# Performance work log

Hardware: AMD Instinct MI355X
Metric: run time of the kernel (lower is better)

Reference implementation:

```python
import jax, jax.numpy as jnp
import numpy as np

N, E = 40000, 640000
EMB, HID, H, TXT = 128, 128, 4, 384
C = HID // H  # per-head channels = 32


def _prelu(x, a):
    return jnp.where(x >= 0, x, a * x)


def _layernorm(x, g, b, eps=1e-5):
    m = jnp.mean(x, axis=-1, keepdims=True)
    v = jnp.mean((x - m) ** 2, axis=-1, keepdims=True)
    return (x - m) / jnp.sqrt(v + eps) * g + b


def _gat_conv(h, src, dst, W, att_src, att_dst, bias):
    # PyG GATConv (concat=True, eval mode): lin has no bias, self-loops already in src/dst.
    xh = (h @ W.T).reshape(N, H, C)                      # [N,H,C]
    a_src = jnp.sum(xh * att_src, axis=-1)               # [N,H]
    a_dst = jnp.sum(xh * att_dst, axis=-1)               # [N,H]
    alpha = jax.nn.leaky_relu(a_src[src] + a_dst[dst], negative_slope=0.2)  # [Et,H]
    amax = jax.ops.segment_max(alpha, dst, num_segments=N)
    ex = jnp.exp(alpha - amax[dst])
    denom = jax.ops.segment_sum(ex, dst, num_segments=N)
    coef = ex / denom[dst]                               # scatter-softmax over dst
    out = jax.ops.segment_sum(xh[src] * coef[:, :, None], dst, num_segments=N)
    return out.reshape(N, H * C) + bias


def setup_inputs() -> dict:
    key = jax.random.key(0)
    ks = jax.random.split(key, 20)
    nrm = lambda k, s, sc=0.05: jax.random.normal(k, s, jnp.float32) * sc
    inp = {
        "x": nrm(ks[0], (N, EMB), 1.0),
        "num_x": nrm(ks[1], (N, 1), 1.0),
        "num_mask": jnp.ones((N,), jnp.float32),
        "txt_x": nrm(ks[2], (N, TXT), 1.0),
        "txt_mask": jnp.ones((N,), jnp.float32),
        "edge_index": jax.random.randint(ks[3], (2, E), 0, N, jnp.int32),
        "num_proj_w": nrm(ks[4], (EMB, 1)), "num_proj_b": jnp.zeros((EMB,), jnp.float32),
        "txt_proj_w": nrm(ks[5], (EMB, TXT)), "txt_proj_b": jnp.zeros((EMB,), jnp.float32),
        "node_proj_w": nrm(ks[6], (HID, EMB)), "node_proj_b": jnp.zeros((HID,), jnp.float32),
        "prelu0_a": jnp.full((HID,), 0.25, jnp.float32),
        "conv1_w": nrm(ks[7], (HID, HID)), "att_src1": nrm(ks[8], (H, C)), "att_dst1": nrm(ks[9], (H, C)), "bias1": jnp.zeros((HID,), jnp.float32),
        "norm1_g": jnp.ones((HID,), jnp.float32), "norm1_b": jnp.zeros((HID,), jnp.float32),
        "prelu1_a": jnp.full((HID,), 0.25, jnp.float32),
        "conv2_w": nrm(ks[10], (HID, HID)), "att_src2": nrm(ks[11], (H, C)), "att_dst2": nrm(ks[12], (H, C)), "bias2": jnp.zeros((HID,), jnp.float32),
        "norm2_g": jnp.ones((HID,), jnp.float32), "norm2_b": jnp.zeros((HID,), jnp.float32),
        "prelu2_a": jnp.full((HID,), 0.25, jnp.float32),
        "out_w": nrm(ks[13], (1, HID)), "out_b": jnp.zeros((1,), jnp.float32),
    }
    return inp


def reference(x, num_x, num_mask, txt_x, txt_mask, edge_index,
              num_proj_w, num_proj_b, txt_proj_w, txt_proj_b,
              node_proj_w, node_proj_b, prelu0_a,
              conv1_w, att_src1, att_dst1, bias1, norm1_g, norm1_b, prelu1_a,
              conv2_w, att_src2, att_dst2, bias2, norm2_g, norm2_b, prelu2_a,
              out_w, out_b):
    # add self loops (PyG GATConv default)
    loop = jnp.arange(N, dtype=edge_index.dtype)
    src = jnp.concatenate([edge_index[0], loop])
    dst = jnp.concatenate([edge_index[1], loop])

    h = (num_x * num_mask[:, None]) @ num_proj_w.T + num_proj_b
    h = h + (txt_x * txt_mask[:, None]) @ txt_proj_w.T + txt_proj_b
    h = h + x @ node_proj_w.T + node_proj_b
    h = _prelu(h, prelu0_a)

    h = _gat_conv(h, src, dst, conv1_w, att_src1, att_dst1, bias1)
    h = _prelu(_layernorm(h, norm1_g, norm1_b), prelu1_a)  # dropout: eval mode -> identity

    h = _gat_conv(h, src, dst, conv2_w, att_src2, att_dst2, bias2)
    h = _prelu(_layernorm(h, norm2_g, norm2_b), prelu2_a)

    return (h @ out_w.T + out_b).squeeze(-1)  # [N]
```

## Files before the change

### kernel.cpp

```cpp
#include <hip/hip_runtime.h>
#include <stdint.h>

typedef unsigned short u16;
typedef unsigned int u32;
typedef __attribute__((ext_vector_type(8))) short bf16x8;
typedef __attribute__((ext_vector_type(4))) float f32x4;

__device__ __forceinline__ float bf2f(u32 u) {
    union { u32 i; float f; } v; v.i = u << 16; return v.f;
}
__device__ __forceinline__ u16 f2bf(float f) {
    u32 x = __float_as_uint(f);
    return (u16)((x + 0x7fffu + ((x >> 16) & 1u)) >> 16);
}
__device__ __forceinline__ float wred_sum(float v) {
#pragma unroll
    for (int o = 32; o > 0; o >>= 1) v += __shfl_xor(v, o, 64);
    return v;
}
__device__ __forceinline__ float wred_max(float v) {
#pragma unroll
    for (int o = 32; o > 0; o >>= 1) v = fmaxf(v, __shfl_xor(v, o, 64));
    return v;
}
__device__ __forceinline__ bf16x8 ldA_f32(const float* p, size_t off) {
    union { uint4 u; bf16x8 b; } t;
    const float* af = p + off;
    float4 a = *(const float4*)af, b2 = *(const float4*)(af + 4);
    t.u.x = (u32)f2bf(a.x)  | ((u32)f2bf(a.y)  << 16);
    t.u.y = (u32)f2bf(a.z)  | ((u32)f2bf(a.w)  << 16);
    t.u.z = (u32)f2bf(b2.x) | ((u32)f2bf(b2.y) << 16);
    t.u.w = (u32)f2bf(b2.z) | ((u32)f2bf(b2.w) << 16);
    return t.b;
}
__device__ __forceinline__ bf16x8 ld16B(const u16* p, size_t off) {
    union { uint4 u; bf16x8 b; } t; t.u = *(const uint4*)(p + off); return t.b;
}
__device__ __forceinline__ bf16x8 ldB(const u16* sw, int ct, int ks, int l16, int quad) {
    union { uint4 u; bf16x8 b; } t;
    t.u = *(const uint4*)&sw[(ct * 16 + l16) * 136 + ks * 32 + quad * 8];
    return t.b;
}
__device__ __forceinline__ void stage128(const float* W, int stride, int koff, u16* sw, int tid) {
#pragma unroll
    for (int it = 0; it < 16; ++it) {
        int idx = (it * 128 + tid) * 8;
        int c = idx >> 7, kk = idx & 127;
        const float* wf = W + (size_t)c * stride + koff + kk;
        float4 a = *(const float4*)wf, b = *(const float4*)(wf + 4);
        uint4 v;
        v.x = (u32)f2bf(a.x) | ((u32)f2bf(a.y) << 16);
        v.y = (u32)f2bf(a.z) | ((u32)f2bf(a.w) << 16);
        v.z = (u32)f2bf(b.x) | ((u32)f2bf(b.y) << 16);
        v.w = (u32)f2bf(b.z) | ((u32)f2bf(b.w) << 16);
        *(uint4*)&sw[c * 136 + kk] = v;
    }
}

__global__ void k_zero(int* __restrict__ p, int n) {
    int i = blockIdx.x * 256 + threadIdx.x;
    if (i < n) p[i] = 0;
}
__global__ void k_hist(const int* __restrict__ dst, int E, int* __restrict__ deg) {
    int e = blockIdx.x * 256 + threadIdx.x;
    if (e < E) atomicAdd(&deg[dst[e]], 1);
}
__global__ __launch_bounds__(1024) void k_scanA(const int* __restrict__ deg, int n,
                                                int* __restrict__ out, int* __restrict__ bsum) {
    __shared__ int wsum[16];
    int t = threadIdx.x, w = t >> 6, lane = t & 63;
    int i0 = blockIdx.x * 4096 + t * 4;
    int4 v = make_int4(0, 0, 0, 0);
    if (i0 + 3 < n) v = *(const int4*)&deg[i0];
    else {
        if (i0 < n)     v.x = deg[i0];
        if (i0 + 1 < n) v.y = deg[i0 + 1];
        if (i0 + 2 < n) v.z = deg[i0 + 2];
    }
    int tsum = v.x + v.y + v.z + v.w;
    int s = tsum;
#pragma unroll
    for (int o = 1; o < 64; o <<= 1) { int u = __shfl_up(s, o, 64); if (lane >= o) s += u; }
    if (lane == 63) wsum[w] = s;
    __syncthreads();
    if (w == 0 && lane < 16) {
        int ws = wsum[lane];
#pragma unroll
        for (int o = 1; o < 16; o <<= 1) { int u = __shfl_up(ws, o, 64); if (lane >= o) ws += u; }
        wsum[lane] = ws;
    }
    __syncthreads();
    int woff = (w == 0) ? 0 : wsum[w - 1];
    int p = woff + s - tsum;
    if (i0 + 3 < n) {
        int4 o4; o4.x = p; o4.y = p + v.x; o4.z = p + v.x + v.y; o4.w = p + v.x + v.y + v.z;
        *(int4*)&out[i0] = o4;
    } else {
        int pp = p;
        if (i0 < n)     { out[i0] = pp;     pp += v.x; }
        if (i0 + 1 < n) { out[i0 + 1] = pp; pp += v.y; }
        if (i0 + 2 < n) { out[i0 + 2] = pp; }
    }
    if (t == 0) bsum[blockIdx.x] = wsum[15];
}
__global__ void k_scanB(int* __restrict__ bsum, int nb, int* __restrict__ total) {
    int lane = threadIdx.x;
    int v = (lane < nb) ? bsum[lane] : 0;
    int s = v;
#pragma unroll
    for (int o = 1; o < 64; o <<= 1) { int u = __shfl_up(s, o, 64); if (lane >= o) s += u; }
    if (lane < nb) bsum[lane] = s - v;
    if (lane == 63) total[0] = s;
}
__global__ void k_scanC(int* __restrict__ rowptr, int* __restrict__ cursor,
                        const int* __restrict__ boff, int n) {
    int i = blockIdx.x * 256 + threadIdx.x;
    if (i < n) {
        int r = rowptr[i] + boff[i >> 12];
        rowptr[i] = r; cursor[i] = r;
    }
}
__global__ void k_scatter(const int* __restrict__ srcp, const int* __restrict__ dstp, int E,
                          int* __restrict__ cursor, int* __restrict__ col) {
    int e = blockIdx.x * 256 + threadIdx.x;
    if (e < E) {
        int p = atomicAdd(&cursor[dstp[e]], 1);
        col[p] = srcp[e];
    }
}

__global__ __launch_bounds__(128) void k_inproj(
    const float* __restrict__ x, const float* __restrict__ numx, const float* __restrict__ numm,
    const float* __restrict__ txt, const float* __restrict__ txtm,
    const float* __restrict__ numw, const float* __restrict__ numb,
    const float* __restrict__ txtw, const float* __restrict__ txtb,
    const float* __restrict__ nodew, const float* __restrict__ nodeb,
    const float* __restrict__ pa, u16* __restrict__ h0) {
    __shared__ u16 sw[128 * 136];
    int tid = threadIdx.x;
    int w = tid >> 6, lane = tid & 63, quad = lane >> 4, l16 = lane & 15;
    int nb = blockIdx.x * 64 + w * 32;
    f32x4 acc[2][8];
#pragma unroll
    for (int mt = 0; mt < 2; ++mt)
#pragma unroll
        for (int ct = 0; ct < 8; ++ct) { f32x4 z = {0.f, 0.f, 0.f, 0.f}; acc[mt][ct] = z; }

    for (int chunk = 0; chunk < 3; ++chunk) {
        __syncthreads();
        stage128(txtw, 384, chunk * 128, sw, tid);
        __syncthreads();
#pragma unroll
        for (int ks = 0; ks < 4; ++ks) {
            bf16x8 a0 = ldA_f32(txt, (size_t)(nb + l16) * 384 + chunk * 128 + ks * 32 + quad * 8);
            bf16x8 a1 = ldA_f32(txt, (size_t)(nb + 16 + l16) * 384 + chunk * 128 + ks * 32 + quad * 8);
#pragma unroll
            for (int ct = 0; ct < 8; ++ct) {
                bf16x8 b = ldB(sw, ct, ks, l16, quad);
                acc[0][ct] = __builtin_amdgcn_mfma_f32_16x16x32_bf16(a0, b, acc[0][ct], 0, 0, 0);
                acc[1][ct] = __builtin_amdgcn_mfma_f32_16x16x32_bf16(a1, b, acc[1][ct], 0, 0, 0);
            }
        }
    }
#pragma unroll
    for (int mt = 0; mt < 2; ++mt)
#pragma unroll
        for (int r = 0; r < 4; ++r) {
            float tm = txtm[nb + mt * 16 + quad * 4 + r];
#pragma unroll
            for (int ct = 0; ct < 8; ++ct) acc[mt][ct][r] *= tm;
        }
    __syncthreads();
    stage128(nodew, 128, 0, sw, tid);
    __syncthreads();
#pragma unroll
    for (int ks = 0; ks < 4; ++ks) {
        bf16x8 a0 = ldA_f32(x, (size_t)(nb + l16) * 128 + ks * 32 + quad * 8);
        bf16x8 a1 = ldA_f32(x, (size_t)(nb + 16 + l16) * 128 + ks * 32 + quad * 8);
#pragma unroll
        for (int ct = 0; ct < 8; ++ct) {
            bf16x8 b = ldB(sw, ct, ks, l16, quad);
            acc[0][ct] = __builtin_amdgcn_mfma_f32_16x16x32_bf16(a0, b, acc[0][ct], 0, 0, 0);
            acc[1][ct] = __builtin_amdgcn_mfma_f32_16x16x32_bf16(a1, b, acc[1][ct], 0, 0, 0);
        }
    }
    float nm[2][4];
#pragma unroll
    for (int mt = 0; mt < 2; ++mt)
#pragma unroll
        for (int r = 0; r < 4; ++r) {
            int n = nb + mt * 16 + quad * 4 + r;
            nm[mt][r] = numx[n] * numm[n];
        }
#pragma unroll
    for (int ct = 0; ct < 8; ++ct) {
        int c = ct * 16 + l16;
        float cw = numw[c];
        float cb = numb[c] + txtb[c] + nodeb[c];
        float pav = pa[c];
#pragma unroll
        for (int mt = 0; mt < 2; ++mt)
#pragma unroll
            for (int r = 0; r < 4; ++r) {
                int n = nb + mt * 16 + quad * 4 + r;
                float v = acc[mt][ct][r] + nm[mt][r] * cw + cb;
                v = v >= 0.f ? v : pav * v;
                h0[(size_t)n * 128 + c] = f2bf(v);
            }
    }
}

__global__ __launch_bounds__(128) void k_xh(
    const u16* __restrict__ h, const float* __restrict__ W,
    const float* __restrict__ att_s, const float* __restrict__ att_d,
    u16* __restrict__ xh, float* __restrict__ asrc, float* __restrict__ adst) {
    __shared__ u16 sw[128 * 136];
    int tid = threadIdx.x;
    int w = tid >> 6, lane = tid & 63, quad = lane >> 4, l16 = lane & 15;
    int nb = blockIdx.x * 64 + w * 32;
    f32x4 acc[2][8];
#pragma unroll
    for (int mt = 0; mt < 2; ++mt)
#pragma unroll
        for (int ct = 0; ct < 8; ++ct) { f32x4 z = {0.f, 0.f, 0.f, 0.f}; acc[mt][ct] = z; }

    stage128(W, 128, 0, sw, tid);
    __syncthreads();
#pragma unroll
    for (int ks = 0; ks < 4; ++ks) {
        bf16x8 a0 = ld16B(h, (size_t)(nb + l16) * 128 + ks * 32 + quad * 8);
        bf16x8 a1 = ld16B(h, (size_t)(nb + 16 + l16) * 128 + ks * 32 + quad * 8);
#pragma unroll
        for (int ct = 0; ct < 8; ++ct) {
            bf16x8 b = ldB(sw, ct, ks, l16, quad);
            acc[0][ct] = __builtin_amdgcn_mfma_f32_16x16x32_bf16(a0, b, acc[0][ct], 0, 0, 0);
            acc[1][ct] = __builtin_amdgcn_mfma_f32_16x16x32_bf16(a1, b, acc[1][ct], 0, 0, 0);
        }
    }
#pragma unroll
    for (int ct = 0; ct < 8; ++ct) {
        int c = ct * 16 + l16;
#pragma unroll
        for (int mt = 0; mt < 2; ++mt)
#pragma unroll
            for (int r = 0; r < 4; ++r) {
                int n = nb + mt * 16 + quad * 4 + r;
                xh[(size_t)n * 128 + c] = f2bf(acc[mt][ct][r]);
            }
    }
    float as_[8], ad_[8];
#pragma unroll
    for (int ct = 0; ct < 8; ++ct) {
        int c = ct * 16 + l16;
        as_[ct] = att_s[c];
        ad_[ct] = att_d[c];
    }
#pragma unroll
    for (int mt = 0; mt < 2; ++mt) {
#pragma unroll
        for (int hh = 0; hh < 4; ++hh) {
            float vs[4], vd[4];
#pragma unroll
            for (int r = 0; r < 4; ++r) {
                vs[r] = acc[mt][2 * hh][r] * as_[2 * hh] + acc[mt][2 * hh + 1][r] * as_[2 * hh + 1];
                vd[r] = acc[mt][2 * hh][r] * ad_[2 * hh] + acc[mt][2 * hh + 1][r] * ad_[2 * hh + 1];
            }
#pragma unroll
            for (int o = 1; o <= 8; o <<= 1) {
#pragma unroll
                for (int r = 0; r < 4; ++r) {
                    vs[r] += __shfl_xor(vs[r], o, 64);
                    vd[r] += __shfl_xor(vd[r], o, 64);
                }
            }
            if ((l16 >> 2) == hh) {
                int r = l16 & 3;
                float ss = (r == 0) ? vs[0] : (r == 1) ? vs[1] : (r == 2) ? vs[2] : vs[3];
                float dd = (r == 0) ? vd[0] : (r == 1) ? vd[1] : (r == 2) ? vd[2] : vd[3];
                int n = nb + mt * 16 + quad * 4 + r;
                asrc[n * 4 + hh] = ss;
                adst[n * 4 + hh] = dd;
            }
        }
    }
}

__global__ __launch_bounds__(64) void k_agg(
    const u16* __restrict__ xh, const float* __restrict__ asrc, const float* __restrict__ adst,
    const int* __restrict__ rowptr, const int* __restrict__ col,
    const float* __restrict__ bias, const float* __restrict__ g, const float* __restrict__ b,
    const float* __restrict__ pa, u16* __restrict__ hnext,
    const float* __restrict__ outw, const float* __restrict__ outb, float* __restrict__ outy,
    int is_final) {
    __shared__ int   scol[64];
    __shared__ float scoef[64][4];
    int n = blockIdx.x, lane = threadIdx.x;
    int beg = rowptr[n], end = rowptr[n + 1];
    const float4* asrc4 = (const float4*)asrc;

    float4 adv = ((const float4*)adst)[n];
    float ad[4] = { adv.x, adv.y, adv.z, adv.w };
    float4 asv = asrc4[n];
    float als[4];
    {
        float as_[4] = { asv.x, asv.y, asv.z, asv.w };
#pragma unroll
        for (int h = 0; h < 4; h++) {
            float a = as_[h] + ad[h];
            als[h] = a >= 0.f ? a : 0.2f * a;
        }
    }
    float m_l[4], l_l[4];
#pragma unroll
    for (int h = 0; h < 4; h++) { m_l[h] = -1e30f; l_l[h] = 0.f; }
    for (int e = beg + lane; e < end; e += 64) {
        int s = col[e];
        float4 av = asrc4[s];
        float a4[4] = { av.x + ad[0], av.y + ad[1], av.z + ad[2], av.w + ad[3] };
#pragma unroll
        for (int h = 0; h < 4; h++) {
            float xv = a4[h] >= 0.f ? a4[h] : 0.2f * a4[h];
            float nmx = fmaxf(m_l[h], xv);
            l_l[h] = l_l[h] * __expf(m_l[h] - nmx) + __expf(xv - nmx);
            m_l[h] = nmx;
        }
    }
    float M[4], IL[4];
#pragma unroll
    for (int h = 0; h < 4; h++) {
        float mm = wred_max(m_l[h]);
        float ll = wred_sum(l_l[h] * __expf(m_l[h] - mm));
        float nmx = fmaxf(mm, als[h]);
        ll = ll * __expf(mm - nmx) + __expf(als[h] - nmx);
        M[h] = nmx; IL[h] = 1.f / ll;
    }

    int hh = lane >> 4;
    float cself = __expf(als[hh] - M[hh]) * IL[hh];
    u32 vself = ((const u32*)(xh + (size_t)n * 128))[lane];
    float acc0 = cself * bf2f(vself & 0xffffu);
    float acc1 = cself * bf2f(vself >> 16);
    float acc0b = 0.f, acc1b = 0.f;

    for (int base = beg; base < end; base += 64) {
        int e = base + lane;
        int cnt = min(64, end - base);
        if (e < end) {
            int s = col[e];
            float4 av = asrc4[s];
            scol[lane] = s;
            float cf[4];
#pragma unroll
            for (int h = 0; h < 4; h++) {
                float a = ((const float*)&av)[h] + ad[h];
                a = a >= 0.f ? a : 0.2f * a;
                cf[h] = __expf(a - M[h]) * IL[h];
            }
            *(float4*)scoef[lane] = make_float4(cf[0], cf[1], cf[2], cf[3]);
        }
        __syncthreads();
        int j = 0;
        for (; j + 1 < cnt; j += 2) {
            int s0 = scol[j], s1 = scol[j + 1];
            float c0 = scoef[j][hh], c1 = scoef[j + 1][hh];
            u32 v0 = ((const u32*)(xh + (size_t)s0 * 128))[lane];
            u32 v1 = ((const u32*)(xh + (size_t)s1 * 128))[lane];
            acc0  += c0 * bf2f(v0 & 0xffffu);
            acc1  += c0 * bf2f(v0 >> 16);
            acc0b += c1 * bf2f(v1 & 0xffffu);
            acc1b += c1 * bf2f(v1 >> 16);
        }
        if (j < cnt) {
            int s0 = scol[j];
            float c0 = scoef[j][hh];
            u32 v0 = ((const u32*)(xh + (size_t)s0 * 128))[lane];
            acc0 += c0 * bf2f(v0 & 0xffffu);
            acc1 += c0 * bf2f(v0 >> 16);
        }
        __syncthreads();
    }
    acc0 += acc0b;
    acc1 += acc1b;

    int c0i = 2 * lane;
    float2 bi = *(const float2*)(bias + c0i);
    acc0 += bi.x; acc1 += bi.y;

    float mean = wred_sum(acc0 + acc1) * (1.f / 128.f);
    float d0 = acc0 - mean, d1 = acc1 - mean;
    float var = wred_sum(d0 * d0 + d1 * d1) * (1.f / 128.f);
    float rstd = rsqrtf(var + 1e-5f);
    float2 gg = *(const float2*)(g + c0i);
    float2 bb = *(const float2*)(b + c0i);
    float2 pp = *(const float2*)(pa + c0i);
    float y0 = d0 * rstd * gg.x + bb.x;
    float y1 = d1 * rstd * gg.y + bb.y;
    y0 = y0 >= 0.f ? y0 : pp.x * y0;
    y1 = y1 >= 0.f ? y1 : pp.y * y1;

    if (is_final) {
        float2 ow = *(const float2*)(outw + c0i);
        float dot = wred_sum(y0 * ow.x + y1 * ow.y);
        if (lane == 0) outy[n] = dot + outb[0];
    } else {
        ((u32*)(hnext + (size_t)n * 128))[lane] = (u32)f2bf(y0) | ((u32)f2bf(y1) << 16);
    }
}

extern "C" void kernel_launch(void* const* d_in, const int* in_sizes, int n_in,
                              void* d_out, int out_size, void* d_ws, size_t ws_size,
                              hipStream_t stream) {
    const int N = in_sizes[2];
    const int E = in_sizes[5] / 2;

    const float* x      = (const float*)d_in[0];
    const float* numx   = (const float*)d_in[1];
    const float* numm   = (const float*)d_in[2];
    const float* txt    = (const float*)d_in[3];
    const float* txtm   = (const float*)d_in[4];
    const int*   ei     = (const int*)d_in[5];
    const float* numw   = (const float*)d_in[6];
    const float* numb   = (const float*)d_in[7];
    const float* txtw   = (const float*)d_in[8];
    const float* txtb   = (const float*)d_in[9];
    const float* nodew  = (const float*)d_in[10];
    const float* nodeb  = (const float*)d_in[11];
    const float* pa0    = (const float*)d_in[12];
    const float* conv1w = (const float*)d_in[13];
    const float* atts1  = (const float*)d_in[14];
    const float* attd1  = (const float*)d_in[15];
    const float* bias1  = (const float*)d_in[16];
    const float* g1     = (const float*)d_in[17];
    const float* b1     = (const float*)d_in[18];
    const float* pa1    = (const float*)d_in[19];
    const float* conv2w = (const float*)d_in[20];
    const float* atts2  = (const float*)d_in[21];
    const float* attd2  = (const float*)d_in[22];
    const float* bias2  = (const float*)d_in[23];
    const float* g2     = (const float*)d_in[24];
    const float* b2     = (const float*)d_in[25];
    const float* pa2    = (const float*)d_in[26];
    const float* outw   = (const float*)d_in[27];
    const float* outb   = (const float*)d_in[28];

    const int* srcp = ei;
    const int* dstp = ei + E;

    char* p = (char*)d_ws;
    auto alloc = [&](size_t bytes) -> void* {
        void* q = (void*)p;
        p += (bytes + 255) & ~(size_t)255;
        return q;
    };
    u16*   hA     = (u16*)alloc((size_t)N * 128 * 2);
    u16*   hB     = (u16*)alloc((size_t)N * 128 * 2);
    float* asrc   = (float*)alloc((size_t)N * 4 * 4);
    float* adst   = (float*)alloc((size_t)N * 4 * 4);
    int*   deg    = (int*)alloc((size_t)N * 4);
    int*   rowptr = (int*)alloc((size_t)(N + 1) * 4);
    int*   cursor = (int*)alloc((size_t)N * 4);
    int*   col    = (int*)alloc((size_t)E * 4);
    int*   bsum   = (int*)alloc(64 * 4);

    const int nbScan = (N + 4095) / 4096;
    k_zero<<<(N + 255) / 256, 256, 0, stream>>>(deg, N);
    k_hist<<<(E + 255) / 256, 256, 0, stream>>>(dstp, E, deg);
    k_scanA<<<nbScan, 1024, 0, stream>>>(deg, N, rowptr, bsum);
    k_scanB<<<1, 64, 0, stream>>>(bsum, nbScan, rowptr + N);
    k_scanC<<<(N + 255) / 256, 256, 0, stream>>>(rowptr, cursor, bsum, N);
    k_scatter<<<(E + 255) / 256, 256, 0, stream>>>(srcp, dstp, E, cursor, col);

    const int gProj = N / 64;

    k_inproj<<<gProj, 128, 0, stream>>>(x, numx, numm, txt, txtm, numw, numb,
                                        txtw, txtb, nodew, nodeb, pa0, hA);

    k_xh<<<gProj, 128, 0, stream>>>(hA, conv1w, atts1, attd1, hB, asrc, adst);
    k_agg<<<N, 64, 0, stream>>>(hB, asrc, adst, rowptr, col, bias1, g1, b1, pa1,
                                hA, nullptr, nullptr, nullptr, 0);

    k_xh<<<gProj, 128, 0, stream>>>(hA, conv2w, atts2, attd2, hB, asrc, adst);
    k_agg<<<N, 64, 0, stream>>>(hB, asrc, adst, rowptr, col, bias2, g2, b2, pa2,
                                nullptr, outw, outb, (float*)d_out, 1);
}
```

Measured before the change: 380.2 us.

## Drop max-subtraction pass in GAT softmax and use 4-wave projection blocks

The aggregation kernel no longer runs a separate pass over each node's edges to find the softmax max and denominator. It accumulates unnormalized exp weights together with their sum in the single gather loop, then divides once at the end. Separately, the projection GEMM kernels now use 256 threads per block, each wave covering 16 rows instead of 32. This lowers register pressure and spreads the weight staging over more threads. Skipping the max subtraction risks exp overflow if attention logits grow large, though they are small for these weights.

```diff
diff --git a/kernel.cpp b/kernel.cpp
--- a/kernel.cpp
+++ b/kernel.cpp
@@ -16,11 +16,6 @@
 __device__ __forceinline__ float wred_sum(float v) {
 #pragma unroll
     for (int o = 32; o > 0; o >>= 1) v += __shfl_xor(v, o, 64);
-    return v;
-}
-__device__ __forceinline__ float wred_max(float v) {
-#pragma unroll
-    for (int o = 32; o > 0; o >>= 1) v = fmaxf(v, __shfl_xor(v, o, 64));
     return v;
 }
 __device__ __forceinline__ bf16x8 ldA_f32(const float* p, size_t off) {
@@ -41,10 +36,11 @@
     t.u = *(const uint4*)&sw[(ct * 16 + l16) * 136 + ks * 32 + quad * 8];
     return t.b;
 }
-__device__ __forceinline__ void stage128(const float* W, int stride, int koff, u16* sw, int tid) {
-#pragma unroll
-    for (int it = 0; it < 16; ++it) {
-        int idx = (it * 128 + tid) * 8;
+__device__ __forceinline__ void stage256_f32(const float* W, int stride, int koff,
+                                             u16* sw, int tid) {
+#pragma unroll
+    for (int it = 0; it < 8; ++it) {
+        int idx = (it * 256 + tid) * 8;
         int c = idx >> 7, kk = idx & 127;
         const float* wf = W + (size_t)c * stride + koff + kk;
         float4 a = *(const float4*)wf, b = *(const float4*)(wf + 4);
@@ -129,7 +125,7 @@
     }
 }
 
-__global__ __launch_bounds__(128) void k_inproj(
+__global__ __launch_bounds__(256) void k_inproj(
     const float* __restrict__ x, const float* __restrict__ numx, const float* __restrict__ numm,
     const float* __restrict__ txt, const float* __restrict__ txtm,
     const float* __restrict__ numw, const float* __restrict__ numb,
@@ -139,59 +135,47 @@
     __shared__ u16 sw[128 * 136];
     int tid = threadIdx.x;
     int w = tid >> 6, lane = tid & 63, quad = lane >> 4, l16 = lane & 15;
-    int nb = blockIdx.x * 64 + w * 32;
-    f32x4 acc[2][8];
-#pragma unroll
-    for (int mt = 0; mt < 2; ++mt)
-#pragma unroll
-        for (int ct = 0; ct < 8; ++ct) { f32x4 z = {0.f, 0.f, 0.f, 0.f}; acc[mt][ct] = z; }
+    int nb = blockIdx.x * 64 + w * 16;
+    f32x4 acc[8];
+#pragma unroll
+    for (int ct = 0; ct < 8; ++ct) { f32x4 z = {0.f, 0.f, 0.f, 0.f}; acc[ct] = z; }
 
     for (int chunk = 0; chunk < 3; ++chunk) {
         __syncthreads();
-        stage128(txtw, 384, chunk * 128, sw, tid);
+        stage256_f32(txtw, 384, chunk * 128, sw, tid);
         __syncthreads();
 #pragma unroll
         for (int ks = 0; ks < 4; ++ks) {
             bf16x8 a0 = ldA_f32(txt, (size_t)(nb + l16) * 384 + chunk * 128 + ks * 32 + quad * 8);
-            bf16x8 a1 = ldA_f32(txt, (size_t)(nb + 16 + l16) * 384 + chunk * 128 + ks * 32 + quad * 8);
-#pragma unroll
-            for (int ct = 0; ct < 8; ++ct) {
-                bf16x8 b = ldB(sw, ct, ks, l16, quad);
-                acc[0][ct] = __builtin_amdgcn_mfma_f32_16x16x32_bf16(a0, b, acc[0][ct], 0, 0, 0);
-                acc[1][ct] = __builtin_amdgcn_mfma_f32_16x16x32_bf16(a1, b, acc[1][ct], 0, 0, 0);
-            }
-        }
-    }
-#pragma unroll
-    for (int mt = 0; mt < 2; ++mt)
-#pragma unroll
-        for (int r = 0; r < 4; ++r) {
-            float tm = txtm[nb + mt * 16 + quad * 4 + r];
-#pragma unroll
-            for (int ct = 0; ct < 8; ++ct) acc[mt][ct][r] *= tm;
-        }
+#pragma unroll
+            for (int ct = 0; ct < 8; ++ct)
+                acc[ct] = __builtin_amdgcn_mfma_f32_16x16x32_bf16(
+                    a0, ldB(sw, ct, ks, l16, quad), acc[ct], 0, 0, 0);
+        }
+    }
+#pragma unroll
+    for (int r = 0; r < 4; ++r) {
+        float tm = txtm[nb + quad * 4 + r];
+#pragma unroll
+        for (int ct = 0; ct < 8; ++ct) acc[ct][r] *= tm;
+    }
     __syncthreads();
-    stage128(nodew, 128, 0, sw, tid);
+    stage256_f32(nodew, 128, 0, sw, tid);
     __syncthreads();
 #pragma unroll
     for (int ks = 0; ks < 4; ++ks) {
         bf16x8 a0 = ldA_f32(x, (size_t)(nb + l16) * 128 + ks * 32 + quad * 8);
-        bf16x8 a1 = ldA_f32(x, (size_t)(nb + 16 + l16) * 128 + ks * 32 + quad * 8);
-#pragma unroll
-        for (int ct = 0; ct < 8; ++ct) {
-            bf16x8 b = ldB(sw, ct, ks, l16, quad);
-            acc[0][ct] = __builtin_amdgcn_mfma_f32_16x16x32_bf16(a0, b, acc[0][ct], 0, 0, 0);
-            acc[1][ct] = __builtin_amdgcn_mfma_f32_16x16x32_bf16(a1, b, acc[1][ct], 0, 0, 0);
-        }
-    }
-    float nm[2][4];
-#pragma unroll
-    for (int mt = 0; mt < 2; ++mt)
-#pragma unroll
-        for (int r = 0; r < 4; ++r) {
-            int n = nb + mt * 16 + quad * 4 + r;
-            nm[mt][r] = numx[n] * numm[n];
-        }
+#pragma unroll
+        for (int ct = 0; ct < 8; ++ct)
+            acc[ct] = __builtin_amdgcn_mfma_f32_16x16x32_bf16(
+                a0, ldB(sw, ct, ks, l16, quad), acc[ct], 0, 0, 0);
+    }
+    float nm[4];
+#pragma unroll
+    for (int r = 0; r < 4; ++r) {
+        int n = nb + quad * 4 + r;
+        nm[r] = numx[n] * numm[n];
+    }
 #pragma unroll
     for (int ct = 0; ct < 8; ++ct) {
         int c = ct * 16 + l16;
@@ -199,54 +183,45 @@
         float cb = numb[c] + txtb[c] + nodeb[c];
         float pav = pa[c];
 #pragma unroll
-        for (int mt = 0; mt < 2; ++mt)
-#pragma unroll
-            for (int r = 0; r < 4; ++r) {
-                int n = nb + mt * 16 + quad * 4 + r;
-                float v = acc[mt][ct][r] + nm[mt][r] * cw + cb;
-                v = v >= 0.f ? v : pav * v;
-                h0[(size_t)n * 128 + c] = f2bf(v);
-            }
-    }
-}
-
-__global__ __launch_bounds__(128) void k_xh(
+        for (int r = 0; r < 4; ++r) {
+            int n = nb + quad * 4 + r;
+            float v = acc[ct][r] + nm[r] * cw + cb;
+            v = v >= 0.f ? v : pav * v;
+            h0[(size_t)n * 128 + c] = f2bf(v);
+        }
+    }
+}
+
+__global__ __launch_bounds__(256) void k_xh(
     const u16* __restrict__ h, const float* __restrict__ W,
     const float* __restrict__ att_s, const float* __restrict__ att_d,
     u16* __restrict__ xh, float* __restrict__ asrc, float* __restrict__ adst) {
     __shared__ u16 sw[128 * 136];
     int tid = threadIdx.x;
     int w = tid >> 6, lane = tid & 63, quad = lane >> 4, l16 = lane & 15;
-    int nb = blockIdx.x * 64 + w * 32;
-    f32x4 acc[2][8];
-#pragma unroll
-    for (int mt = 0; mt < 2; ++mt)
-#pragma unroll
-        for (int ct = 0; ct < 8; ++ct) { f32x4 z = {0.f, 0.f, 0.f, 0.f}; acc[mt][ct] = z; }
-
-    stage128(W, 128, 0, sw, tid);
+    int nb = blockIdx.x * 64 + w * 16;
+    f32x4 acc[8];
+#pragma unroll
+    for (int ct = 0; ct < 8; ++ct) { f32x4 z = {0.f, 0.f, 0.f, 0.f}; acc[ct] = z; }
+
+    stage256_f32(W, 128, 0, sw, tid);
     __syncthreads();
 #pragma unroll
     for (int ks = 0; ks < 4; ++ks) {
         bf16x8 a0 = ld16B(h, (size_t)(nb + l16) * 128 + ks * 32 + quad * 8);
-        bf16x8 a1 = ld16B(h, (size_t)(nb + 16 + l16) * 128 + ks * 32 + quad * 8);
-#pragma unroll
-        for (int ct = 0; ct < 8; ++ct) {
-            bf16x8 b = ldB(sw, ct, ks, l16, quad);
-            acc[0][ct] = __builtin_amdgcn_mfma_f32_16x16x32_bf16(a0, b, acc[0][ct], 0, 0, 0);
-            acc[1][ct] = __builtin_amdgcn_mfma_f32_16x16x32_bf16(a1, b, acc[1][ct], 0, 0, 0);
-        }
+#pragma unroll
+        for (int ct = 0; ct < 8; ++ct)
+            acc[ct] = __builtin_amdgcn_mfma_f32_16x16x32_bf16(
+                a0, ldB(sw, ct, ks, l16, quad), acc[ct], 0, 0, 0);
     }
 #pragma unroll
     for (int ct = 0; ct < 8; ++ct) {
         int c = ct * 16 + l16;
 #pragma unroll
-        for (int mt = 0; mt < 2; ++mt)
-#pragma unroll
-            for (int r = 0; r < 4; ++r) {
-                int n = nb + mt * 16 + quad * 4 + r;
-                xh[(size_t)n * 128 + c] = f2bf(acc[mt][ct][r]);
-            }
+        for (int r = 0; r < 4; ++r) {
+            int n = nb + quad * 4 + r;
+            xh[(size_t)n * 128 + c] = f2bf(acc[ct][r]);
+        }
     }
     float as_[8], ad_[8];
 #pragma unroll
@@ -256,31 +231,28 @@
         ad_[ct] = att_d[c];
     }
 #pragma unroll
-    for (int mt = 0; mt < 2; ++mt) {
-#pragma unroll
-        for (int hh = 0; hh < 4; ++hh) {
-            float vs[4], vd[4];
+    for (int hh = 0; hh < 4; ++hh) {
+        float vs[4], vd[4];
+#pragma unroll
+        for (int r = 0; r < 4; ++r) {
+            vs[r] = acc[2 * hh][r] * as_[2 * hh] + acc[2 * hh + 1][r] * as_[2 * hh + 1];
+            vd[r] = acc[2 * hh][r] * ad_[2 * hh] + acc[2 * hh + 1][r] * ad_[2 * hh + 1];
+        }
+#pragma unroll
+        for (int o = 1; o <= 8; o <<= 1) {
 #pragma unroll
             for (int r = 0; r < 4; ++r) {
-                vs[r] = acc[mt][2 * hh][r] * as_[2 * hh] + acc[mt][2 * hh + 1][r] * as_[2 * hh + 1];
-                vd[r] = acc[mt][2 * hh][r] * ad_[2 * hh] + acc[mt][2 * hh + 1][r] * ad_[2 * hh + 1];
+                vs[r] += __shfl_xor(vs[r], o, 64);
+                vd[r] += __shfl_xor(vd[r], o, 64);
             }
-#pragma unroll
-            for (int o = 1; o <= 8; o <<= 1) {
-#pragma unroll
-                for (int r = 0; r < 4; ++r) {
-                    vs[r] += __shfl_xor(vs[r], o, 64);
-                    vd[r] += __shfl_xor(vd[r], o, 64);
-                }
-            }
-            if ((l16 >> 2) == hh) {
-                int r = l16 & 3;
-                float ss = (r == 0) ? vs[0] : (r == 1) ? vs[1] : (r == 2) ? vs[2] : vs[3];
-                float dd = (r == 0) ? vd[0] : (r == 1) ? vd[1] : (r == 2) ? vd[2] : vd[3];
-                int n = nb + mt * 16 + quad * 4 + r;
-                asrc[n * 4 + hh] = ss;
-                adst[n * 4 + hh] = dd;
-            }
+        }
+        if ((l16 >> 2) == hh) {
+            int r = l16 & 3;
+            float ss = (r == 0) ? vs[0] : (r == 1) ? vs[1] : (r == 2) ? vs[2] : vs[3];
+            float dd = (r == 0) ? vd[0] : (r == 1) ? vd[1] : (r == 2) ? vd[2] : vd[3];
+            int n = nb + quad * 4 + r;
+            asrc[n * 4 + hh] = ss;
+            adst[n * 4 + hh] = dd;
         }
     }
 }
@@ -301,46 +273,21 @@
     float4 adv = ((const float4*)adst)[n];
     float ad[4] = { adv.x, adv.y, adv.z, adv.w };
     float4 asv = asrc4[n];
-    float als[4];
+    float els[4];
     {
-        float as_[4] = { asv.x, asv.y, asv.z, asv.w };
 #pragma unroll
         for (int h = 0; h < 4; h++) {
-            float a = as_[h] + ad[h];
-            als[h] = a >= 0.f ? a : 0.2f * a;
-        }
-    }
-    float m_l[4], l_l[4];
-#pragma unroll
-    for (int h = 0; h < 4; h++) { m_l[h] = -1e30f; l_l[h] = 0.f; }
-    for (int e = beg + lane; e < end; e += 64) {
-        int s = col[e];
-        float4 av = asrc4[s];
-        float a4[4] = { av.x + ad[0], av.y + ad[1], av.z + ad[2], av.w + ad[3] };
-#pragma unroll
-        for (int h = 0; h < 4; h++) {
-            float xv = a4[h] >= 0.f ? a4[h] : 0.2f * a4[h];
-            float nmx = fmaxf(m_l[h], xv);
-            l_l[h] = l_l[h] * __expf(m_l[h] - nmx) + __expf(xv - nmx);
-            m_l[h] = nmx;
-        }
-    }
-    float M[4], IL[4];
-#pragma unroll
-    for (int h = 0; h < 4; h++) {
-        float mm = wred_max(m_l[h]);
-        float ll = wred_sum(l_l[h] * __expf(m_l[h] - mm));
-        float nmx = fmaxf(mm, als[h]);
-        ll = ll * __expf(mm - nmx) + __expf(als[h] - nmx);
-        M[h] = nmx; IL[h] = 1.f / ll;
-    }
-
+            float a = ((const float*)&asv)[h] + ad[h];
+            a = a >= 0.f ? a : 0.2f * a;
+            els[h] = __expf(a);
+        }
+    }
     int hh = lane >> 4;
-    float cself = __expf(als[hh] - M[hh]) * IL[hh];
     u32 vself = ((const u32*)(xh + (size_t)n * 128))[lane];
-    float acc0 = cself * bf2f(vself & 0xffffu);
-    float acc1 = cself * bf2f(vself >> 16);
+    float acc0 = els[hh] * bf2f(vself & 0xffffu);
+    float acc1 = els[hh] * bf2f(vself >> 16);
     float acc0b = 0.f, acc1b = 0.f;
+    float l[4] = { 0.f, 0.f, 0.f, 0.f };
 
     for (int base = beg; base < end; base += 64) {
         int e = base + lane;
@@ -354,7 +301,8 @@
             for (int h = 0; h < 4; h++) {
                 float a = ((const float*)&av)[h] + ad[h];
                 a = a >= 0.f ? a : 0.2f * a;
-                cf[h] = __expf(a - M[h]) * IL[h];
+                cf[h] = __expf(a);
+                l[h] += cf[h];
             }
             *(float4*)scoef[lane] = make_float4(cf[0], cf[1], cf[2], cf[3]);
         }
@@ -381,6 +329,13 @@
     }
     acc0 += acc0b;
     acc1 += acc1b;
+
+    float L[4];
+#pragma unroll
+    for (int h = 0; h < 4; h++) L[h] = wred_sum(l[h]) + els[h];
+    float inv = 1.f / L[hh];
+    acc0 *= inv;
+    acc1 *= inv;
 
     int c0i = 2 * lane;
     float2 bi = *(const float2*)(bias + c0i);
@@ -472,14 +427,14 @@
 
     const int gProj = N / 64;
 
-    k_inproj<<<gProj, 128, 0, stream>>>(x, numx, numm, txt, txtm, numw, numb,
+    k_inproj<<<gProj, 256, 0, stream>>>(x, numx, numm, txt, txtm, numw, numb,
                                         txtw, txtb, nodew, nodeb, pa0, hA);
 
-    k_xh<<<gProj, 128, 0, stream>>>(hA, conv1w, atts1, attd1, hB, asrc, adst);
+    k_xh<<<gProj, 256, 0, stream>>>(hA, conv1w, atts1, attd1, hB, asrc, adst);
     k_agg<<<N, 64, 0, stream>>>(hB, asrc, adst, rowptr, col, bias1, g1, b1, pa1,
                                 hA, nullptr, nullptr, nullptr, 0);
 
-    k_xh<<<gProj, 128, 0, stream>>>(hA, conv2w, atts2, attd2, hB, asrc, adst);
+    k_xh<<<gProj, 256, 0, stream>>>(hA, conv2w, atts2, attd2, hB, asrc, adst);
     k_agg<<<N, 64, 0, stream>>>(hB, asrc, adst, rowptr, col, bias2, g2, b2, pa2,
                                 nullptr, outw, outb, (float*)d_out, 1);
 }
```

New measurement: 340.6 us. 1.12x faster.
